# Kernel optimization log

Hardware: AMD Instinct MI355X
Metric: run time of the kernel (lower is better)

Reference implementation:

```python
import jax, jax.numpy as jnp
import numpy as np

B, LQ, LK, DK, DV = 32, 128, 4096, 256, 256


def setup_inputs() -> dict:
    key = jax.random.key(0)
    k1, k2, k3, k4, k5 = jax.random.split(key, 5)
    return {
        "query": jax.random.normal(k1, (B, LQ, DK), dtype=jnp.float32),
        "query_lengths": jax.random.randint(k2, (B,), 1, LQ, dtype=jnp.int32),
        "keys": jax.random.normal(k3, (B, LK, DK), dtype=jnp.float32),
        "values": jax.random.normal(k4, (B, LK, DV), dtype=jnp.float32),
        "mask": jax.random.randint(k5, (B, LK), 0, 2, dtype=jnp.int32),  # 1 = masked out
    }


def reference(query, query_lengths, keys, values, mask):
    # zero query positions beyond each example's length (torch: mask_query masked_fill 0)
    q_valid = jnp.arange(query.shape[1])[None, :] < query_lengths[:, None]  # [B, Lq]
    query = jnp.where(q_valid[:, :, None], query, 0.0)
    # zero masked key/value timesteps (torch mask: 1 -> masked)
    kv_valid = (mask == 0)[:, :, None]  # [B, Lk, 1]
    keys = jnp.where(kv_valid, keys, 0.0)
    values = jnp.where(kv_valid, values, 0.0)
    # attention scores [B, Lq, Lk]
    weights = jnp.einsum("bqd,bkd->bqk", query, keys)
    # exact-zero scores (masked rows/cols) -> -inf, matching torch weights==0.0 fill
    weights = jnp.where(weights == 0.0, -jnp.inf, weights)
    weights = jax.nn.softmax(weights, axis=-1)
    # rows that were all -inf produce NaN -> cleaned to 0
    weights = jnp.where(jnp.isnan(weights), 0.0, weights)
    attended = jnp.einsum("bqk,bkv->bqv", weights, values)  # [B, Lq, Dv]
    return jnp.mean(attended, axis=1)  # [B, Dv]
```

## Files before the change

### kernel.cpp

```cpp
#include <hip/hip_runtime.h>
#include <hip/hip_fp16.h>
#include <stdint.h>

#define NB  32
#define NLQ 128
#define NLK 4096
#define NDK 256
#define NDV 256
#define KT  16
#define SPLITS 8
#define MINSPLITS 4

typedef _Float16 f16;
typedef _Float16 f16x4 __attribute__((ext_vector_type(4)));
typedef _Float16 f16x8 __attribute__((ext_vector_type(8)));
typedef float    f32x4 __attribute__((ext_vector_type(4)));

__global__ __launch_bounds__(256) void fvta_part1(
    const float* __restrict__ q_, const float* __restrict__ k_,
    const float* __restrict__ v_, const int* __restrict__ mask_,
    f16* __restrict__ accw, float* __restrict__ mlw)
{
    __shared__ __align__(16) f16 KA[2][KT * NDK];
    __shared__ int MK[NLK / MINSPLITS];

    const int tid = threadIdx.x, w = tid >> 6, lane = tid & 63;
    const int l15 = lane & 15, lhi = lane >> 4;
    const int s = blockIdx.x, b = blockIdx.y, qh = blockIdx.z, S = gridDim.x;
    const int slice = NLK / S, nt = slice / KT, kbase = s * slice;
    const float NEG = -__builtin_inff();

    const float* kb = k_ + ((size_t)b * NLK + kbase) * NDK;
    const float* vb = v_ + ((size_t)b * NLK + kbase) * NDV;
    const int*   mb = mask_ + b * NLK + kbase;

    for (int i = tid; i < slice; i += 256) MK[i] = mb[i];

    f16x8 qf[8];
    {
        const float* qrow = q_ + ((size_t)b * NLQ + qh * 64 + w * 16 + l15) * NDK + lhi * 8;
        #pragma unroll
        for (int kd = 0; kd < 8; ++kd) {
            f32x4 x = *(const f32x4*)(qrow + kd * 32);
            f32x4 y = *(const f32x4*)(qrow + kd * 32 + 4);
            f16x8 f;
            f[0]=(f16)x[0]; f[1]=(f16)x[1]; f[2]=(f16)x[2]; f[3]=(f16)x[3];
            f[4]=(f16)y[0]; f[5]=(f16)y[1]; f[6]=(f16)y[2]; f[7]=(f16)y[3];
            qf[kd] = f;
        }
    }

    f32x4 accu[16];
    #pragma unroll
    for (int i = 0; i < 16; ++i) accu[i] = (f32x4){0.f, 0.f, 0.f, 0.f};
    float m_run = NEG, l_run = 0.f;

    f32x4 ks[4];

    auto stage = [&](f16* KAb) {
        #pragma unroll
        for (int r = 0; r < 4; ++r) {
            const int idx = r * 256 + tid;
            const int kk  = idx >> 6;
            const int d   = (idx & 63) * 4;
            const int e   = kk * NDK + (d ^ (kk << 3));
            f32x4 x = ks[r];
            f16x4 hh; hh[0]=(f16)x[0]; hh[1]=(f16)x[1]; hh[2]=(f16)x[2]; hh[3]=(f16)x[3];
            *(f16x4*)(KAb + e) = hh;
        }
    };

    #pragma unroll
    for (int r = 0; r < 4; ++r)
        ks[r] = *(const f32x4*)(kb + (r * 256 + tid) * 4);
    stage(KA[0]);
    __syncthreads();

    const int swz = l15 << 3;

    for (int t = 0; t < nt; ++t) {
        const int cur = t & 1;
        if (t + 1 < nt) {
            const float* ksrc = kb + (size_t)(t + 1) * KT * NDK;
            #pragma unroll
            for (int r = 0; r < 4; ++r)
                ks[r] = *(const f32x4*)(ksrc + (r * 256 + tid) * 4);
        }
        const int k0 = t * KT;

        f32x4 s4 = (f32x4){0.f,0.f,0.f,0.f};
        {
            const f16* kp = &KA[cur][l15 * NDK];
            #pragma unroll
            for (int kd = 0; kd < 8; ++kd) {
                const int col = (kd * 32 + lhi * 8) ^ swz;
                f16x8 kf = *(const f16x8*)(kp + col);
                s4 = __builtin_amdgcn_mfma_f32_16x16x32_f16(kf, qf[kd], s4, 0, 0, 0);
            }
        }

        const int4 m4 = *(const int4*)(MK + k0 + lhi * 4);
        float sa[4];
        sa[0] = m4.x ? NEG : s4[0]; sa[1] = m4.y ? NEG : s4[1];
        sa[2] = m4.z ? NEG : s4[2]; sa[3] = m4.w ? NEG : s4[3];

        float tmax = fmaxf(fmaxf(sa[0], sa[1]), fmaxf(sa[2], sa[3]));
        tmax = fmaxf(tmax, __shfl_xor(tmax, 16, 64));
        tmax = fmaxf(tmax, __shfl_xor(tmax, 32, 64));
        const float mnew = fmaxf(m_run, tmax);
        const bool  dead = (mnew == NEG);
        const float scale = dead ? 1.f : __expf(m_run - mnew);
        float p4[4];
        #pragma unroll
        for (int j = 0; j < 4; ++j) p4[j] = dead ? 0.f : __expf(sa[j] - mnew);
        float ps = (p4[0] + p4[1]) + (p4[2] + p4[3]);
        ps += __shfl_xor(ps, 16, 64);
        ps += __shfl_xor(ps, 32, 64);
        l_run = l_run * scale + ps;
        m_run = mnew;

        f16x4 pa;
        pa[0]=(f16)p4[0]; pa[1]=(f16)p4[1]; pa[2]=(f16)p4[2]; pa[3]=(f16)p4[3];

        if (!__all(scale == 1.f)) {
            float scj[4];
            #pragma unroll
            for (int j = 0; j < 4; ++j) scj[j] = __shfl(scale, lhi * 4 + j, 64);
            #pragma unroll
            for (int d = 0; d < 16; ++d) {
                accu[d][0] *= scj[0]; accu[d][1] *= scj[1];
                accu[d][2] *= scj[2]; accu[d][3] *= scj[3];
            }
        }

        {
            const float* vr = vb + (size_t)(k0 + lhi * 4) * NDV + l15;
            #pragma unroll
            for (int dg = 0; dg < 4; ++dg) {
                float tv[4][4];
                #pragma unroll
                for (int dd = 0; dd < 4; ++dd) {
                    const float* vc = vr + (dg * 4 + dd) * 16;
                    tv[dd][0] = vc[0];
                    tv[dd][1] = vc[1 * NDV];
                    tv[dd][2] = vc[2 * NDV];
                    tv[dd][3] = vc[3 * NDV];
                }
                #pragma unroll
                for (int dd = 0; dd < 4; ++dd) {
                    f16x4 vf;
                    vf[0]=(f16)tv[dd][0]; vf[1]=(f16)tv[dd][1];
                    vf[2]=(f16)tv[dd][2]; vf[3]=(f16)tv[dd][3];
                    accu[dg * 4 + dd] = __builtin_amdgcn_mfma_f32_16x16x16f16(
                        pa, vf, accu[dg * 4 + dd], 0, 0, 0);
                }
            }
        }

        if (t + 1 < nt) stage(KA[cur ^ 1]);
        __syncthreads();
    }

    const size_t base = (size_t)(b * S + s) * NLQ + qh * 64 + w * 16;
    #pragma unroll
    for (int j = 0; j < 4; ++j) {
        f16* dst = accw + (base + lhi * 4 + j) * NDV + l15;
        #pragma unroll
        for (int d = 0; d < 16; ++d) dst[d * 16] = (f16)accu[d][j];
    }
    if (lane < 16) {
        mlw[(base + lane) * 2]     = m_run;
        mlw[(base + lane) * 2 + 1] = l_run;
    }
}

__global__ __launch_bounds__(256) void fvta_merge(
    const f16* __restrict__ accw, const float* __restrict__ mlw,
    const int* __restrict__ qlen_, float* __restrict__ out_, int S)
{
    __shared__ float fac[8][SPLITS + 1];
    const int qc = blockIdx.x, b = blockIdx.y, tid = threadIdx.x;
    const int len = qlen_[b];
    const float NEG = -__builtin_inff();

    if (tid < 8) {
        const int q = qc * 8 + tid;
        if (q < len) {
            float gm = NEG;
            for (int ss = 0; ss < S; ++ss)
                gm = fmaxf(gm, mlw[((size_t)(b * S + ss) * NLQ + q) * 2]);
            float L = 0.f;
            for (int ss = 0; ss < S; ++ss) {
                const float m = mlw[((size_t)(b * S + ss) * NLQ + q) * 2];
                const float l = mlw[((size_t)(b * S + ss) * NLQ + q) * 2 + 1];
                if (m != NEG) L += l * __expf(m - gm);
            }
            for (int ss = 0; ss < S; ++ss) {
                const float m = mlw[((size_t)(b * S + ss) * NLQ + q) * 2];
                fac[tid][ss] = (gm != NEG && L > 0.f && m != NEG)
                             ? __expf(m - gm) / L : 0.f;
            }
        } else {
            for (int ss = 0; ss < S; ++ss) fac[tid][ss] = 0.f;
        }
    }
    __syncthreads();

    float sum = 0.f;
    for (int qq = 0; qq < 8; ++qq) {
        const int q = qc * 8 + qq;
        for (int ss = 0; ss < S; ++ss) {
            const float f = fac[qq][ss];
            if (f != 0.f)
                sum += (float)accw[((size_t)(b * S + ss) * NLQ + q) * NDV + tid] * f;
        }
    }
    atomicAdd(&out_[b * NDV + tid], sum * (1.f / NLQ));
}

extern "C" void kernel_launch(void* const* d_in, const int* in_sizes, int n_in,
                              void* d_out, int out_size, void* d_ws, size_t ws_size,
                              hipStream_t stream) {
    const float* q    = (const float*)d_in[0];
    const int*   qlen = (const int*)d_in[1];
    const float* k    = (const float*)d_in[2];
    const float* v    = (const float*)d_in[3];
    const int*   mask = (const int*)d_in[4];
    float* out = (float*)d_out;

    int S = SPLITS;
    while (S > MINSPLITS &&
           ((size_t)NB * S * NLQ * NDV * 2 + (size_t)NB * S * NLQ * 8) > ws_size)
        S >>= 1;
    f16*   accw = (f16*)d_ws;
    float* mlw  = (float*)((char*)d_ws + (size_t)NB * S * NLQ * NDV * 2);

    hipMemsetAsync(out, 0, (size_t)out_size * sizeof(float), stream);
    dim3 g1(S, NB, 2);
    fvta_part1<<<g1, 256, 0, stream>>>(q, k, v, mask, accw, mlw);
    dim3 g2(NLQ / 8, NB);
    fvta_merge<<<g2, 256, 0, stream>>>(accw, mlw, qlen, out, S);
}
```

Baseline: 123.3 us.

## Split DV across wave pairs with 512-thread blocks and shared-memory query tile

Blocks grow to 512 threads (8 waves). Each pair of waves shares a 16-row query group and splits the value dimension in half, which halves the accumulator registers per wave. The query tile is converted to f16 and staged once in swizzled LDS instead of held in registers. Each wave still recomputes the QK scores and softmax redundantly, and the block now reads Q from LDS on every tile. This trades more LDS traffic and duplicated score work for lower register pressure and more waves per block.

```diff
diff --git a/kernel.cpp b/kernel.cpp
--- a/kernel.cpp
+++ b/kernel.cpp
@@ -16,17 +16,22 @@
 typedef _Float16 f16x8 __attribute__((ext_vector_type(8)));
 typedef float    f32x4 __attribute__((ext_vector_type(4)));
 
-__global__ __launch_bounds__(256) void fvta_part1(
+__global__ __launch_bounds__(512) void fvta_part1(
     const float* __restrict__ q_, const float* __restrict__ k_,
     const float* __restrict__ v_, const int* __restrict__ mask_,
     f16* __restrict__ accw, float* __restrict__ mlw)
 {
     __shared__ __align__(16) f16 KA[2][KT * NDK];
+    __shared__ __align__(16) f16 QA[64 * NDK];
     __shared__ int MK[NLK / MINSPLITS];
 
     const int tid = threadIdx.x, w = tid >> 6, lane = tid & 63;
     const int l15 = lane & 15, lhi = lane >> 4;
-    const int s = blockIdx.x, b = blockIdx.y, qh = blockIdx.z, S = gridDim.x;
+    const int qsub = w >> 1;
+    const int dvh  = w & 1;
+    const int x = blockIdx.x, b = blockIdx.y;
+    const int S = gridDim.x >> 1;
+    const int s = x >> 1, qz = x & 1;
     const int slice = NLK / S, nt = slice / KT, kbase = s * slice;
     const float NEG = -__builtin_inff();
 
@@ -34,45 +39,44 @@
     const float* vb = v_ + ((size_t)b * NLK + kbase) * NDV;
     const int*   mb = mask_ + b * NLK + kbase;
 
-    for (int i = tid; i < slice; i += 256) MK[i] = mb[i];
-
-    f16x8 qf[8];
+    for (int i = tid; i < slice; i += 512) MK[i] = mb[i];
+
     {
-        const float* qrow = q_ + ((size_t)b * NLQ + qh * 64 + w * 16 + l15) * NDK + lhi * 8;
-        #pragma unroll
-        for (int kd = 0; kd < 8; ++kd) {
-            f32x4 x = *(const f32x4*)(qrow + kd * 32);
-            f32x4 y = *(const f32x4*)(qrow + kd * 32 + 4);
-            f16x8 f;
-            f[0]=(f16)x[0]; f[1]=(f16)x[1]; f[2]=(f16)x[2]; f[3]=(f16)x[3];
-            f[4]=(f16)y[0]; f[5]=(f16)y[1]; f[6]=(f16)y[2]; f[7]=(f16)y[3];
-            qf[kd] = f;
-        }
-    }
-
-    f32x4 accu[16];
+        const float* qsrc = q_ + ((size_t)b * NLQ + qz * 64) * NDK;
+        #pragma unroll
+        for (int r = 0; r < 8; ++r) {
+            const int idx = r * 512 + tid;
+            const int qq  = idx >> 6;
+            const int d   = (idx & 63) * 4;
+            f32x4 xv = *(const f32x4*)(qsrc + qq * NDK + d);
+            f16x4 hh; hh[0]=(f16)xv[0]; hh[1]=(f16)xv[1]; hh[2]=(f16)xv[2]; hh[3]=(f16)xv[3];
+            *(f16x4*)(QA + qq * NDK + (d ^ ((qq & 15) << 3))) = hh;
+        }
+    }
+
+    f32x4 accu[8];
     #pragma unroll
-    for (int i = 0; i < 16; ++i) accu[i] = (f32x4){0.f, 0.f, 0.f, 0.f};
+    for (int i = 0; i < 8; ++i) accu[i] = (f32x4){0.f, 0.f, 0.f, 0.f};
     float m_run = NEG, l_run = 0.f;
 
-    f32x4 ks[4];
+    f32x4 ks[2];
 
     auto stage = [&](f16* KAb) {
         #pragma unroll
-        for (int r = 0; r < 4; ++r) {
-            const int idx = r * 256 + tid;
+        for (int r = 0; r < 2; ++r) {
+            const int idx = r * 512 + tid;
             const int kk  = idx >> 6;
             const int d   = (idx & 63) * 4;
             const int e   = kk * NDK + (d ^ (kk << 3));
-            f32x4 x = ks[r];
-            f16x4 hh; hh[0]=(f16)x[0]; hh[1]=(f16)x[1]; hh[2]=(f16)x[2]; hh[3]=(f16)x[3];
+            f32x4 xv = ks[r];
+            f16x4 hh; hh[0]=(f16)xv[0]; hh[1]=(f16)xv[1]; hh[2]=(f16)xv[2]; hh[3]=(f16)xv[3];
             *(f16x4*)(KAb + e) = hh;
         }
     };
 
     #pragma unroll
-    for (int r = 0; r < 4; ++r)
-        ks[r] = *(const f32x4*)(kb + (r * 256 + tid) * 4);
+    for (int r = 0; r < 2; ++r)
+        ks[r] = *(const f32x4*)(kb + (r * 512 + tid) * 4);
     stage(KA[0]);
     __syncthreads();
 
@@ -83,19 +87,21 @@
         if (t + 1 < nt) {
             const float* ksrc = kb + (size_t)(t + 1) * KT * NDK;
             #pragma unroll
-            for (int r = 0; r < 4; ++r)
-                ks[r] = *(const f32x4*)(ksrc + (r * 256 + tid) * 4);
+            for (int r = 0; r < 2; ++r)
+                ks[r] = *(const f32x4*)(ksrc + (r * 512 + tid) * 4);
         }
         const int k0 = t * KT;
 
         f32x4 s4 = (f32x4){0.f,0.f,0.f,0.f};
         {
             const f16* kp = &KA[cur][l15 * NDK];
+            const f16* qp = &QA[(qsub * 16 + l15) * NDK];
             #pragma unroll
             for (int kd = 0; kd < 8; ++kd) {
                 const int col = (kd * 32 + lhi * 8) ^ swz;
                 f16x8 kf = *(const f16x8*)(kp + col);
-                s4 = __builtin_amdgcn_mfma_f32_16x16x32_f16(kf, qf[kd], s4, 0, 0, 0);
+                f16x8 qv = *(const f16x8*)(qp + col);
+                s4 = __builtin_amdgcn_mfma_f32_16x16x32_f16(kf, qv, s4, 0, 0, 0);
             }
         }
 
@@ -127,16 +133,16 @@
             #pragma unroll
             for (int j = 0; j < 4; ++j) scj[j] = __shfl(scale, lhi * 4 + j, 64);
             #pragma unroll
-            for (int d = 0; d < 16; ++d) {
+            for (int d = 0; d < 8; ++d) {
                 accu[d][0] *= scj[0]; accu[d][1] *= scj[1];
                 accu[d][2] *= scj[2]; accu[d][3] *= scj[3];
             }
         }
 
         {
-            const float* vr = vb + (size_t)(k0 + lhi * 4) * NDV + l15;
-            #pragma unroll
-            for (int dg = 0; dg < 4; ++dg) {
+            const float* vr = vb + (size_t)(k0 + lhi * 4) * NDV + dvh * 128 + l15;
+            #pragma unroll
+            for (int dg = 0; dg < 2; ++dg) {
                 float tv[4][4];
                 #pragma unroll
                 for (int dd = 0; dd < 4; ++dd) {
@@ -161,14 +167,14 @@
         __syncthreads();
     }
 
-    const size_t base = (size_t)(b * S + s) * NLQ + qh * 64 + w * 16;
+    const size_t base = (size_t)(b * S + s) * NLQ + qz * 64 + qsub * 16;
     #pragma unroll
     for (int j = 0; j < 4; ++j) {
-        f16* dst = accw + (base + lhi * 4 + j) * NDV + l15;
-        #pragma unroll
-        for (int d = 0; d < 16; ++d) dst[d * 16] = (f16)accu[d][j];
-    }
-    if (lane < 16) {
+        f16* dst = accw + (base + lhi * 4 + j) * NDV + dvh * 128 + l15;
+        #pragma unroll
+        for (int d = 0; d < 8; ++d) dst[d * 16] = (f16)accu[d][j];
+    }
+    if (dvh == 0 && lane < 16) {
         mlw[(base + lane) * 2]     = m_run;
         mlw[(base + lane) * 2 + 1] = l_run;
     }
@@ -236,8 +242,8 @@
     float* mlw  = (float*)((char*)d_ws + (size_t)NB * S * NLQ * NDV * 2);
 
     hipMemsetAsync(out, 0, (size_t)out_size * sizeof(float), stream);
-    dim3 g1(S, NB, 2);
-    fvta_part1<<<g1, 256, 0, stream>>>(q, k, v, mask, accw, mlw);
+    dim3 g1(2 * S, NB);
+    fvta_part1<<<g1, 512, 0, stream>>>(q, k, v, mask, accw, mlw);
     dim3 g2(NLQ / 8, NB);
     fvta_merge<<<g2, 256, 0, stream>>>(accw, mlw, qlen, out, S);
 }
```

Measured after the change: 124.6 us. Within noise of the previous version (+1.0%).
